# Kernel optimization log

Measured on AMD Instinct MI355X. Metric: run time of the kernel, lower is better.

## Reference

```python
import jax, jax.numpy as jnp
import numpy as np

# Geometry constants matching PointLoss.__init__ defaults
FOV_H = 360.0   # horizontal FOV (deg)
FOV_VU = 3.0    # upper vertical FOV (deg)
DH = 0.5        # delta_h
DV = 0.5        # delta_v
PROJ_H = 52     # int(26 / 0.5)
PROJ_W = 720    # int(360 / 0.5)
THETAC = 0.5    # confidence threshold
LAMDA = 1.0     # fov-loss weight
ANGRATE = 1.0   # anglelossrate
EPS = 1e-8


def setup_inputs() -> dict:
    key = jax.random.key(0)
    ks = jax.random.split(key, 10)
    B, H, W = 64, PROJ_H, PROJ_W
    return {
        "vertexmap_proj": jax.random.normal(ks[0], (B, H, W, 3), jnp.float32),
        "normalmap_proj": jax.random.normal(ks[1], (B, H, W, 3), jnp.float32),
        "uncertainty": jax.random.uniform(ks[2], (B, H, W), jnp.float32),
        "now_normalmap": jax.random.normal(ks[3], (B, H, W, 3), jnp.float32),
        "now_confidencemap": jax.random.uniform(ks[4], (B, H, W), jnp.float32),
        "last_normalmap": jax.random.normal(ks[5], (B, H, W, 3), jnp.float32),
        "last_vertexmap": jax.random.normal(ks[6], (B, H, W, 3), jnp.float32),
        "sx": jnp.zeros((1,), jnp.float32),
        "sq": jnp.zeros((1,), jnp.float32),
        "now_maskmap": jax.random.randint(ks[7], (B, H, W), 0, 2, jnp.int32),
        "last_maskmap": jax.random.randint(ks[8], (B, H, W), 0, 2, jnp.int32),
    }


def _gather_proj(m, flat_idx, B, H, W):
    """Gather pixels of m [B,H,W,(C)] at flat index [B,H,W] -> same shape as m."""
    if m.ndim == 3:
        mf = m.reshape(B, H * W)
        return jnp.take_along_axis(mf, flat_idx.reshape(B, H * W), axis=1).reshape(B, H, W)
    C = m.shape[-1]
    mf = m.reshape(B, H * W, C)
    idx = jnp.broadcast_to(flat_idx.reshape(B, H * W, 1), (B, H * W, C))
    return jnp.take_along_axis(mf, idx, axis=1).reshape(B, H, W, C)


def reference(vertexmap_proj, normalmap_proj, uncertainty, now_normalmap,
              now_confidencemap, last_normalmap, last_vertexmap, sx, sq,
              now_maskmap, last_maskmap):
    B, H, W, _ = vertexmap_proj.shape
    v = vertexmap_proj

    # mask of valid current pixels: maskmap > 0 and normal non-zero
    mask0 = (now_maskmap > 0) & (jnp.sum(jnp.abs(now_normalmap), -1) != 0)

    # spherical re-projection (movegrid=True)
    depth = jnp.sqrt(jnp.sum(v * v, -1) + EPS)
    yaw = jnp.arctan2(v[..., 1], v[..., 0]) * (180.0 / np.pi)
    pitch = jnp.arcsin(jnp.clip(v[..., 2] / depth, -1.0, 1.0)) * (180.0 / np.pi)
    proj_x = (FOV_H / 2 - yaw) / DH
    proj_y = (FOV_VU - pitch) / DV

    # fov loss = masked mse(proj, clamp(proj)) (F.mse_loss default mean)
    m0 = mask0.astype(v.dtype)
    n0 = jnp.maximum(jnp.sum(m0), 1.0)
    fovloss = (jnp.sum(m0 * (proj_x - jnp.clip(proj_x, 0, W - 1)) ** 2)
               + jnp.sum(m0 * (proj_y - jnp.clip(proj_y, 0, H - 1)) ** 2)) / n0

    prx = jnp.round(proj_x)
    pry = jnp.round(proj_y)
    inb = (prx >= 0) & (prx < W) & (pry >= 0) & (pry < H)
    prxi = jnp.clip(prx, 0, W - 1).astype(jnp.int32)
    pryi = jnp.clip(pry, 0, H - 1).astype(jnp.int32)
    flat = pryi * W + prxi  # [B,H,W]

    nl = _gather_proj(last_normalmap, flat, B, H, W)   # last normal at projected pixel
    vl = _gather_proj(last_vertexmap, flat, B, H, W)   # last vertex at projected pixel
    lm = _gather_proj(last_maskmap, flat, B, H, W)

    lastmask = (lm > 0) & (jnp.sum(jnp.abs(nl), -1) != 0)
    mask = mask0 & inb & lastmask & (now_confidencemap >= THETAC)
    m = mask.astype(v.dtype)
    n = jnp.maximum(jnp.sum(m), 1.0)

    # point-to-plane ICP residual, uncertainty-weighted L1
    r = jnp.sum(nl * (v - vl), -1)
    icploss = jnp.sum(m * uncertainty * jnp.abs(r)) / n

    # angular loss: 1 - |cos(angle between normals)|
    nn = normalmap_proj
    cosang = jnp.abs(jnp.sum(nl * nn, -1)) / jnp.sqrt(
        jnp.sum(nl * nl, -1) * jnp.sum(nn * nn, -1) + EPS)
    angloss = jnp.sum(m * uncertainty * (1.0 - cosang)) / n

    sx0, sq0 = sx[0], sq[0]
    total = (jnp.exp(-sx0) * icploss + sx0
             + ANGRATE * jnp.exp(-sq0) * angloss + sq0
             + LAMDA * fovloss)
    return total
```

## Files before the change

### kernel.cpp

```cpp
#include <hip/hip_runtime.h>
#include <math.h>


namespace {
constexpr int B_ = 64, H_ = 52, W_ = 720;
constexpr int HW_ = H_ * W_;
constexpr int NPIX = B_ * HW_;
constexpr int QPI  = HW_ / 4;
constexpr int NQUAD = NPIX / 4;
constexpr int NTHREADS = 256;
constexpr int NBLOCKS = NQUAD / NTHREADS;
constexpr float EPSF = 1e-8f;
constexpr float RAD2DEG = 57.29577951308232f;
}
static_assert(NBLOCKS * NTHREADS == NQUAD, "grid must tile quads exactly");

__global__ __launch_bounds__(NTHREADS) void pointloss_main(
    const float* __restrict__ v,
    const float* __restrict__ nrm,
    const float* __restrict__ unc,
    const float* __restrict__ nown,
    const float* __restrict__ conf,
    const float* __restrict__ lastn,
    const float* __restrict__ lastv,
    const int*   __restrict__ nowm,
    const int*   __restrict__ lastm,
    float* __restrict__ partials)
{
    float s_m0 = 0.f, s_fov = 0.f, s_m = 0.f, s_icp = 0.f, s_ang = 0.f;

    const float4* __restrict__ v4 = (const float4*)v;
    const float4* __restrict__ n4 = (const float4*)nown;
    const float4* __restrict__ r4 = (const float4*)nrm;
    const float4* __restrict__ u4 = (const float4*)unc;
    const int4*   __restrict__ m4 = (const int4*)nowm;
    const float4* __restrict__ c4 = (const float4*)conf;

    const int q  = blockIdx.x * NTHREADS + threadIdx.x;
    const int gbase = (q / QPI) * HW_;

    const float4 va = v4[3*q+0], vb = v4[3*q+1], vc = v4[3*q+2];
    const float4 na = n4[3*q+0], nb = n4[3*q+1], nc = n4[3*q+2];
    const int4   mm = m4[q];
    const float4 cf = c4[q];

    const float vx[4] = {va.x, va.w, vb.z, vc.y};
    const float vy[4] = {va.y, vb.x, vb.w, vc.z};
    const float vz[4] = {va.z, vb.y, vc.x, vc.w};
    const float ax[4] = {na.x, na.w, nb.z, nc.y};
    const float ay[4] = {na.y, nb.x, nb.w, nc.z};
    const float az[4] = {na.z, nb.y, nc.x, nc.w};
    const int   mk[4] = {mm.x, mm.y, mm.z, mm.w};
    const float cv[4] = {cf.x, cf.y, cf.z, cf.w};

    bool g[4];
    int  gi[4];
    #pragma unroll
    for (int j = 0; j < 4; ++j) {
        const bool mask0 = (mk[j] > 0) &&
            ((fabsf(ax[j]) + fabsf(ay[j]) + fabsf(az[j])) != 0.0f);

        const float depth = sqrtf(vx[j]*vx[j] + vy[j]*vy[j] + vz[j]*vz[j] + EPSF);
        const float yaw   = atan2f(vy[j], vx[j]) * RAD2DEG;
        const float pitch = asinf(fminf(fmaxf(vz[j] / depth, -1.f), 1.f)) * RAD2DEG;
        const float px = (180.0f - yaw) * 2.0f;
        const float py = (3.0f - pitch) * 2.0f;

        if (mask0) {
            const float dx = px - fminf(fmaxf(px, 0.f), (float)(W_ - 1));
            const float dy = py - fminf(fmaxf(py, 0.f), (float)(H_ - 1));
            s_m0  += 1.0f;
            s_fov += dx*dx + dy*dy;
        }

        const float prx = rintf(px), pry = rintf(py);
        const bool inb = (prx >= 0.f) && (prx < (float)W_) &&
                         (pry >= 0.f) && (pry < (float)H_);
        g[j]  = mask0 && inb && (cv[j] >= 0.5f);
        gi[j] = g[j] ? (gbase + (int)pry * W_ + (int)prx) : 0;
    }
    const bool anyg = g[0] | g[1] | g[2] | g[3];

    float4 ra = {0,0,0,0}, rb = {0,0,0,0}, rc = {0,0,0,0}, uq = {0,0,0,0};
    if (anyg) {
        ra = r4[3*q+0]; rb = r4[3*q+1]; rc = r4[3*q+2];
        uq = u4[q];
    }
    float lx[4] = {0,0,0,0}, ly[4] = {0,0,0,0}, lz[4] = {0,0,0,0};
    float wx[4] = {0,0,0,0}, wy[4] = {0,0,0,0}, wz[4] = {0,0,0,0};
    int   lm[4] = {0,0,0,0};
    #pragma unroll
    for (int j = 0; j < 4; ++j) {
        if (g[j]) {
            const int gi3 = 3 * gi[j];
            lx[j] = lastn[gi3+0]; ly[j] = lastn[gi3+1]; lz[j] = lastn[gi3+2];
            lm[j] = lastm[gi[j]];
            wx[j] = lastv[gi3+0]; wy[j] = lastv[gi3+1]; wz[j] = lastv[gi3+2];
        }
    }

    const float nx[4] = {ra.x, ra.w, rb.z, rc.y};
    const float ny[4] = {ra.y, rb.x, rb.w, rc.z};
    const float nz[4] = {ra.z, rb.y, rc.x, rc.w};
    const float uu[4] = {uq.x, uq.y, uq.z, uq.w};

    #pragma unroll
    for (int j = 0; j < 4; ++j) {
        if (g[j] && (lm[j] > 0) &&
            ((fabsf(lx[j]) + fabsf(ly[j]) + fabsf(lz[j])) != 0.f)) {
            const float r  = lx[j]*(vx[j]-wx[j]) + ly[j]*(vy[j]-wy[j])
                           + lz[j]*(vz[j]-wz[j]);
            const float dt = lx[j]*nx[j] + ly[j]*ny[j] + lz[j]*nz[j];
            const float den = (lx[j]*lx[j] + ly[j]*ly[j] + lz[j]*lz[j]) *
                              (nx[j]*nx[j] + ny[j]*ny[j] + nz[j]*nz[j]) + EPSF;
            const float cosang = fabsf(dt) * rsqrtf(den);
            s_m   += 1.0f;
            s_icp += uu[j] * fabsf(r);
            s_ang += uu[j] * (1.0f - cosang);
        }
    }

    #pragma unroll
    for (int off = 32; off > 0; off >>= 1) {
        s_m0  += __shfl_down(s_m0,  off);
        s_fov += __shfl_down(s_fov, off);
        s_m   += __shfl_down(s_m,   off);
        s_icp += __shfl_down(s_icp, off);
        s_ang += __shfl_down(s_ang, off);
    }
    __shared__ float red[NTHREADS / 64][5];
    const int lane = threadIdx.x & 63;
    const int wv   = threadIdx.x >> 6;
    if (lane == 0) {
        red[wv][0] = s_m0;  red[wv][1] = s_fov; red[wv][2] = s_m;
        red[wv][3] = s_icp; red[wv][4] = s_ang;
    }
    __syncthreads();
    if (threadIdx.x == 0) {
        float t[5] = {0.f, 0.f, 0.f, 0.f, 0.f};
        for (int w2 = 0; w2 < NTHREADS / 64; ++w2)
            for (int c = 0; c < 5; ++c) t[c] += red[w2][c];
        float* o = partials + blockIdx.x * 5;
        for (int c = 0; c < 5; ++c) o[c] = t[c];
    }
}

__global__ __launch_bounds__(256) void pointloss_finalize(
    const float* __restrict__ partials,
    const float* __restrict__ sx,
    const float* __restrict__ sq,
    float* __restrict__ out)
{
    double a0 = 0, a1 = 0, a2 = 0, a3 = 0, a4 = 0;
    for (int i = threadIdx.x; i < NBLOCKS; i += 256) {
        const float* pp = partials + i * 5;
        a0 += (double)pp[0]; a1 += (double)pp[1]; a2 += (double)pp[2];
        a3 += (double)pp[3]; a4 += (double)pp[4];
    }
    #pragma unroll
    for (int off = 32; off > 0; off >>= 1) {
        a0 += __shfl_down(a0, off);
        a1 += __shfl_down(a1, off);
        a2 += __shfl_down(a2, off);
        a3 += __shfl_down(a3, off);
        a4 += __shfl_down(a4, off);
    }
    __shared__ double red[4][5];
    const int lane = threadIdx.x & 63;
    const int wv   = threadIdx.x >> 6;
    if (lane == 0) {
        red[wv][0] = a0; red[wv][1] = a1; red[wv][2] = a2;
        red[wv][3] = a3; red[wv][4] = a4;
    }
    __syncthreads();
    if (threadIdx.x == 0) {
        double t[5] = {0, 0, 0, 0, 0};
        for (int w2 = 0; w2 < 4; ++w2)
            for (int c = 0; c < 5; ++c) t[c] += red[w2][c];
        const double n0 = fmax(t[0], 1.0);
        const double n  = fmax(t[2], 1.0);
        const double sx0 = (double)sx[0], sq0 = (double)sq[0];
        const double total = exp(-sx0) * (t[3] / n) + sx0
                           + exp(-sq0) * (t[4] / n) + sq0
                           + t[1] / n0;
        out[0] = (float)total;
    }
}

extern "C" void kernel_launch(void* const* d_in, const int* in_sizes, int n_in,
                              void* d_out, int out_size, void* d_ws, size_t ws_size,
                              hipStream_t stream) {
    const float* v     = (const float*)d_in[0];
    const float* nrm   = (const float*)d_in[1];
    const float* unc   = (const float*)d_in[2];
    const float* nown  = (const float*)d_in[3];
    const float* conf  = (const float*)d_in[4];
    const float* lastn = (const float*)d_in[5];
    const float* lastv = (const float*)d_in[6];
    const float* sx    = (const float*)d_in[7];
    const float* sq    = (const float*)d_in[8];
    const int*   nowm  = (const int*)d_in[9];
    const int*   lastm = (const int*)d_in[10];

    float* partials = (float*)d_ws;

    pointloss_main<<<NBLOCKS, NTHREADS, 0, stream>>>(
        v, nrm, unc, nown, conf, lastn, lastv, nowm, lastm, partials);
    pointloss_finalize<<<1, 256, 0, stream>>>(partials, sx, sq, (float*)d_out);
}
```

Before: 197.3 us.

## Process four quads per thread with register prefetch of next quad's streamed inputs

Each thread now handles four quads strided across the grid and loads the next quad's vertex, normal, mask and confidence vectors before computing the current one. This software pipelining is meant to hide global-load latency behind the trig-heavy projection math, and it cuts the block count and partial-sum count by four. The cost is higher register pressure, which may lower occupancy, and less parallelism to hide the latency of the data-dependent gathers.

```diff
diff --git a/kernel.cpp b/kernel.cpp
--- a/kernel.cpp
+++ b/kernel.cpp
@@ -9,11 +9,20 @@
 constexpr int QPI  = HW_ / 4;
 constexpr int NQUAD = NPIX / 4;
 constexpr int NTHREADS = 256;
-constexpr int NBLOCKS = NQUAD / NTHREADS;
+constexpr int QPT = 4;
+constexpr int NBLOCKS = NQUAD / (NTHREADS * QPT);
+constexpr int TSTRIDE = NBLOCKS * NTHREADS;
 constexpr float EPSF = 1e-8f;
 constexpr float RAD2DEG = 57.29577951308232f;
 }
-static_assert(NBLOCKS * NTHREADS == NQUAD, "grid must tile quads exactly");
+static_assert(NBLOCKS * NTHREADS * QPT == NQUAD, "grid must tile quads exactly");
+
+struct Stream {
+    float4 va, vb, vc;
+    float4 na, nb, nc;
+    int4   mm;
+    float4 cf;
+};
 
 __global__ __launch_bounds__(NTHREADS) void pointloss_main(
     const float* __restrict__ v,
@@ -36,88 +45,105 @@
     const int4*   __restrict__ m4 = (const int4*)nowm;
     const float4* __restrict__ c4 = (const float4*)conf;
 
-    const int q  = blockIdx.x * NTHREADS + threadIdx.x;
-    const int gbase = (q / QPI) * HW_;
-
-    const float4 va = v4[3*q+0], vb = v4[3*q+1], vc = v4[3*q+2];
-    const float4 na = n4[3*q+0], nb = n4[3*q+1], nc = n4[3*q+2];
-    const int4   mm = m4[q];
-    const float4 cf = c4[q];
-
-    const float vx[4] = {va.x, va.w, vb.z, vc.y};
-    const float vy[4] = {va.y, vb.x, vb.w, vc.z};
-    const float vz[4] = {va.z, vb.y, vc.x, vc.w};
-    const float ax[4] = {na.x, na.w, nb.z, nc.y};
-    const float ay[4] = {na.y, nb.x, nb.w, nc.z};
-    const float az[4] = {na.z, nb.y, nc.x, nc.w};
-    const int   mk[4] = {mm.x, mm.y, mm.z, mm.w};
-    const float cv[4] = {cf.x, cf.y, cf.z, cf.w};
-
-    bool g[4];
-    int  gi[4];
+    const int tid = blockIdx.x * NTHREADS + threadIdx.x;
+
+    auto ld = [&](int q) {
+        Stream s;
+        s.va = v4[3*q+0]; s.vb = v4[3*q+1]; s.vc = v4[3*q+2];
+        s.na = n4[3*q+0]; s.nb = n4[3*q+1]; s.nc = n4[3*q+2];
+        s.mm = m4[q];
+        s.cf = c4[q];
+        return s;
+    };
+
+    Stream s = ld(tid);
+
     #pragma unroll
-    for (int j = 0; j < 4; ++j) {
-        const bool mask0 = (mk[j] > 0) &&
-            ((fabsf(ax[j]) + fabsf(ay[j]) + fabsf(az[j])) != 0.0f);
-
-        const float depth = sqrtf(vx[j]*vx[j] + vy[j]*vy[j] + vz[j]*vz[j] + EPSF);
-        const float yaw   = atan2f(vy[j], vx[j]) * RAD2DEG;
-        const float pitch = asinf(fminf(fmaxf(vz[j] / depth, -1.f), 1.f)) * RAD2DEG;
-        const float px = (180.0f - yaw) * 2.0f;
-        const float py = (3.0f - pitch) * 2.0f;
-
-        if (mask0) {
-            const float dx = px - fminf(fmaxf(px, 0.f), (float)(W_ - 1));
-            const float dy = py - fminf(fmaxf(py, 0.f), (float)(H_ - 1));
-            s_m0  += 1.0f;
-            s_fov += dx*dx + dy*dy;
-        }
-
-        const float prx = rintf(px), pry = rintf(py);
-        const bool inb = (prx >= 0.f) && (prx < (float)W_) &&
-                         (pry >= 0.f) && (pry < (float)H_);
-        g[j]  = mask0 && inb && (cv[j] >= 0.5f);
-        gi[j] = g[j] ? (gbase + (int)pry * W_ + (int)prx) : 0;
-    }
-    const bool anyg = g[0] | g[1] | g[2] | g[3];
-
-    float4 ra = {0,0,0,0}, rb = {0,0,0,0}, rc = {0,0,0,0}, uq = {0,0,0,0};
-    if (anyg) {
-        ra = r4[3*q+0]; rb = r4[3*q+1]; rc = r4[3*q+2];
-        uq = u4[q];
-    }
-    float lx[4] = {0,0,0,0}, ly[4] = {0,0,0,0}, lz[4] = {0,0,0,0};
-    float wx[4] = {0,0,0,0}, wy[4] = {0,0,0,0}, wz[4] = {0,0,0,0};
-    int   lm[4] = {0,0,0,0};
-    #pragma unroll
-    for (int j = 0; j < 4; ++j) {
-        if (g[j]) {
-            const int gi3 = 3 * gi[j];
-            lx[j] = lastn[gi3+0]; ly[j] = lastn[gi3+1]; lz[j] = lastn[gi3+2];
-            lm[j] = lastm[gi[j]];
-            wx[j] = lastv[gi3+0]; wy[j] = lastv[gi3+1]; wz[j] = lastv[gi3+2];
-        }
-    }
-
-    const float nx[4] = {ra.x, ra.w, rb.z, rc.y};
-    const float ny[4] = {ra.y, rb.x, rb.w, rc.z};
-    const float nz[4] = {ra.z, rb.y, rc.x, rc.w};
-    const float uu[4] = {uq.x, uq.y, uq.z, uq.w};
-
-    #pragma unroll
-    for (int j = 0; j < 4; ++j) {
-        if (g[j] && (lm[j] > 0) &&
-            ((fabsf(lx[j]) + fabsf(ly[j]) + fabsf(lz[j])) != 0.f)) {
-            const float r  = lx[j]*(vx[j]-wx[j]) + ly[j]*(vy[j]-wy[j])
-                           + lz[j]*(vz[j]-wz[j]);
-            const float dt = lx[j]*nx[j] + ly[j]*ny[j] + lz[j]*nz[j];
-            const float den = (lx[j]*lx[j] + ly[j]*ly[j] + lz[j]*lz[j]) *
-                              (nx[j]*nx[j] + ny[j]*ny[j] + nz[j]*nz[j]) + EPSF;
-            const float cosang = fabsf(dt) * rsqrtf(den);
-            s_m   += 1.0f;
-            s_icp += uu[j] * fabsf(r);
-            s_ang += uu[j] * (1.0f - cosang);
-        }
+    for (int it = 0; it < QPT; ++it) {
+        const int q = tid + it * TSTRIDE;
+
+        Stream snext;
+        if (it < QPT - 1) snext = ld(q + TSTRIDE);
+
+        const int gbase = (q / QPI) * HW_;
+
+        const float vx[4] = {s.va.x, s.va.w, s.vb.z, s.vc.y};
+        const float vy[4] = {s.va.y, s.vb.x, s.vb.w, s.vc.z};
+        const float vz[4] = {s.va.z, s.vb.y, s.vc.x, s.vc.w};
+        const float ax[4] = {s.na.x, s.na.w, s.nb.z, s.nc.y};
+        const float ay[4] = {s.na.y, s.nb.x, s.nb.w, s.nc.z};
+        const float az[4] = {s.na.z, s.nb.y, s.nc.x, s.nc.w};
+        const int   mk[4] = {s.mm.x, s.mm.y, s.mm.z, s.mm.w};
+        const float cv[4] = {s.cf.x, s.cf.y, s.cf.z, s.cf.w};
+
+        bool g[4];
+        int  gi[4];
+        #pragma unroll
+        for (int j = 0; j < 4; ++j) {
+            const bool mask0 = (mk[j] > 0) &&
+                ((fabsf(ax[j]) + fabsf(ay[j]) + fabsf(az[j])) != 0.0f);
+
+            const float depth = sqrtf(vx[j]*vx[j] + vy[j]*vy[j] + vz[j]*vz[j] + EPSF);
+            const float yaw   = atan2f(vy[j], vx[j]) * RAD2DEG;
+            const float pitch = asinf(fminf(fmaxf(vz[j] / depth, -1.f), 1.f)) * RAD2DEG;
+            const float px = (180.0f - yaw) * 2.0f;
+            const float py = (3.0f - pitch) * 2.0f;
+
+            if (mask0) {
+                const float dx = px - fminf(fmaxf(px, 0.f), (float)(W_ - 1));
+                const float dy = py - fminf(fmaxf(py, 0.f), (float)(H_ - 1));
+                s_m0  += 1.0f;
+                s_fov += dx*dx + dy*dy;
+            }
+
+            const float prx = rintf(px), pry = rintf(py);
+            const bool inb = (prx >= 0.f) && (prx < (float)W_) &&
+                             (pry >= 0.f) && (pry < (float)H_);
+            g[j]  = mask0 && inb && (cv[j] >= 0.5f);
+            gi[j] = g[j] ? (gbase + (int)pry * W_ + (int)prx) : 0;
+        }
+        const bool anyg = g[0] | g[1] | g[2] | g[3];
+
+        float4 ra = {0,0,0,0}, rb = {0,0,0,0}, rc = {0,0,0,0}, uq = {0,0,0,0};
+        if (anyg) {
+            ra = r4[3*q+0]; rb = r4[3*q+1]; rc = r4[3*q+2];
+            uq = u4[q];
+        }
+        float lx[4] = {0,0,0,0}, ly[4] = {0,0,0,0}, lz[4] = {0,0,0,0};
+        float wx[4] = {0,0,0,0}, wy[4] = {0,0,0,0}, wz[4] = {0,0,0,0};
+        int   lm[4] = {0,0,0,0};
+        #pragma unroll
+        for (int j = 0; j < 4; ++j) {
+            if (g[j]) {
+                const int gi3 = 3 * gi[j];
+                lx[j] = lastn[gi3+0]; ly[j] = lastn[gi3+1]; lz[j] = lastn[gi3+2];
+                lm[j] = lastm[gi[j]];
+                wx[j] = lastv[gi3+0]; wy[j] = lastv[gi3+1]; wz[j] = lastv[gi3+2];
+            }
+        }
+
+        const float nx[4] = {ra.x, ra.w, rb.z, rc.y};
+        const float ny[4] = {ra.y, rb.x, rb.w, rc.z};
+        const float nz[4] = {ra.z, rb.y, rc.x, rc.w};
+        const float uu[4] = {uq.x, uq.y, uq.z, uq.w};
+
+        #pragma unroll
+        for (int j = 0; j < 4; ++j) {
+            if (g[j] && (lm[j] > 0) &&
+                ((fabsf(lx[j]) + fabsf(ly[j]) + fabsf(lz[j])) != 0.f)) {
+                const float r  = lx[j]*(vx[j]-wx[j]) + ly[j]*(vy[j]-wy[j])
+                               + lz[j]*(vz[j]-wz[j]);
+                const float dt = lx[j]*nx[j] + ly[j]*ny[j] + lz[j]*nz[j];
+                const float den = (lx[j]*lx[j] + ly[j]*ly[j] + lz[j]*lz[j]) *
+                                  (nx[j]*nx[j] + ny[j]*ny[j] + nz[j]*nz[j]) + EPSF;
+                const float cosang = fabsf(dt) * rsqrtf(den);
+                s_m   += 1.0f;
+                s_icp += uu[j] * fabsf(r);
+                s_ang += uu[j] * (1.0f - cosang);
+            }
+        }
+
+        s = snext;
     }
 
     #pragma unroll
```

After: 199.1 us. About the same (+0.9%).

## Compact valid pixels into a workspace queue and gather last-frame data separately

Applied to the files above, without the earlier changes.

The main kernel no longer does the divergent random gathers from the last-frame maps. Instead it uses wave ballots and one atomic per wave to append compact 32-byte records for valid pixels to a workspace buffer. A second grid-stride kernel reads those records, performs the gathers and computes the ICP and angle partial sums, and the finalize kernel merges both sets of partials. This aims to remove lane divergence and wasted gather slots in the main pass. In exchange it adds a memset, an extra launch and extra write/read traffic, and records beyond the workspace capacity are silently dropped.

```diff
diff --git a/kernel.cpp b/kernel.cpp
--- a/kernel.cpp
+++ b/kernel.cpp
@@ -8,26 +8,33 @@
 constexpr int NPIX = B_ * HW_;
 constexpr int QPI  = HW_ / 4;
 constexpr int NQUAD = NPIX / 4;
-constexpr int NTHREADS = 256;
-constexpr int NBLOCKS = NQUAD / NTHREADS;
+constexpr int NT = 256;
+constexpr int NB1 = NQUAD / NT;
+constexpr int NB2 = 1024;
 constexpr float EPSF = 1e-8f;
 constexpr float RAD2DEG = 57.29577951308232f;
-}
-static_assert(NBLOCKS * NTHREADS == NQUAD, "grid must tile quads exactly");
-
-__global__ __launch_bounds__(NTHREADS) void pointloss_main(
+
+constexpr size_t WS_COUNTER = 0;
+constexpr size_t WS_P1      = 16;
+constexpr size_t WS_P2      = 20480;
+constexpr size_t WS_RECS    = 65536;
+}
+static_assert(NB1 * NT == NQUAD, "grid must tile quads exactly");
+
+
+__global__ __launch_bounds__(NT) void pointloss_main(
     const float* __restrict__ v,
     const float* __restrict__ nrm,
     const float* __restrict__ unc,
     const float* __restrict__ nown,
     const float* __restrict__ conf,
-    const float* __restrict__ lastn,
-    const float* __restrict__ lastv,
     const int*   __restrict__ nowm,
-    const int*   __restrict__ lastm,
-    float* __restrict__ partials)
+    unsigned int* __restrict__ counter,
+    float* __restrict__ p1,
+    float4* __restrict__ recs,
+    int cap)
 {
-    float s_m0 = 0.f, s_fov = 0.f, s_m = 0.f, s_icp = 0.f, s_ang = 0.f;
+    float s_m0 = 0.f, s_fov = 0.f;
 
     const float4* __restrict__ v4 = (const float4*)v;
     const float4* __restrict__ n4 = (const float4*)nown;
@@ -36,7 +43,7 @@
     const int4*   __restrict__ m4 = (const int4*)nowm;
     const float4* __restrict__ c4 = (const float4*)conf;
 
-    const int q  = blockIdx.x * NTHREADS + threadIdx.x;
+    const int q = blockIdx.x * NT + threadIdx.x;
     const int gbase = (q / QPI) * HW_;
 
     const float4 va = v4[3*q+0], vb = v4[3*q+1], vc = v4[3*q+2];
@@ -86,76 +93,136 @@
         ra = r4[3*q+0]; rb = r4[3*q+1]; rc = r4[3*q+2];
         uq = u4[q];
     }
-    float lx[4] = {0,0,0,0}, ly[4] = {0,0,0,0}, lz[4] = {0,0,0,0};
-    float wx[4] = {0,0,0,0}, wy[4] = {0,0,0,0}, wz[4] = {0,0,0,0};
-    int   lm[4] = {0,0,0,0};
-    #pragma unroll
-    for (int j = 0; j < 4; ++j) {
-        if (g[j]) {
-            const int gi3 = 3 * gi[j];
-            lx[j] = lastn[gi3+0]; ly[j] = lastn[gi3+1]; lz[j] = lastn[gi3+2];
-            lm[j] = lastm[gi[j]];
-            wx[j] = lastv[gi3+0]; wy[j] = lastv[gi3+1]; wz[j] = lastv[gi3+2];
-        }
-    }
-
     const float nx[4] = {ra.x, ra.w, rb.z, rc.y};
     const float ny[4] = {ra.y, rb.x, rb.w, rc.z};
     const float nz[4] = {ra.z, rb.y, rc.x, rc.w};
     const float uu[4] = {uq.x, uq.y, uq.z, uq.w};
 
+    const int lane = threadIdx.x & 63;
+    const unsigned long long lt = ((unsigned long long)1 << lane) - 1ull;
+    unsigned long long bal[4];
+    int tj[4], tot = 0;
     #pragma unroll
     for (int j = 0; j < 4; ++j) {
-        if (g[j] && (lm[j] > 0) &&
-            ((fabsf(lx[j]) + fabsf(ly[j]) + fabsf(lz[j])) != 0.f)) {
-            const float r  = lx[j]*(vx[j]-wx[j]) + ly[j]*(vy[j]-wy[j])
-                           + lz[j]*(vz[j]-wz[j]);
-            const float dt = lx[j]*nx[j] + ly[j]*ny[j] + lz[j]*nz[j];
-            const float den = (lx[j]*lx[j] + ly[j]*ly[j] + lz[j]*lz[j]) *
-                              (nx[j]*nx[j] + ny[j]*ny[j] + nz[j]*nz[j]) + EPSF;
+        bal[j] = __ballot(g[j]);
+        tj[j]  = __popcll(bal[j]);
+        tot   += tj[j];
+    }
+    int base = 0;
+    if (lane == 0 && tot > 0)
+        base = (int)atomicAdd(counter, (unsigned int)tot);
+    base = __shfl(base, 0);
+
+    int off = base;
+    #pragma unroll
+    for (int j = 0; j < 4; ++j) {
+        if (g[j]) {
+            const int idx = off + __popcll(bal[j] & lt);
+            if (idx < cap) {
+                float4 r0, r1;
+                r0.x = __int_as_float(gi[j]);
+                r0.y = uu[j]; r0.z = vx[j]; r0.w = vy[j];
+                r1.x = vz[j]; r1.y = nx[j]; r1.z = ny[j]; r1.w = nz[j];
+                recs[2*idx+0] = r0;
+                recs[2*idx+1] = r1;
+            }
+        }
+        off += tj[j];
+    }
+
+    #pragma unroll
+    for (int o = 32; o > 0; o >>= 1) {
+        s_m0  += __shfl_down(s_m0,  o);
+        s_fov += __shfl_down(s_fov, o);
+    }
+    __shared__ float red[NT / 64][2];
+    const int wv = threadIdx.x >> 6;
+    if (lane == 0) { red[wv][0] = s_m0; red[wv][1] = s_fov; }
+    __syncthreads();
+    if (threadIdx.x == 0) {
+        float t0 = 0.f, t1 = 0.f;
+        for (int w2 = 0; w2 < NT / 64; ++w2) { t0 += red[w2][0]; t1 += red[w2][1]; }
+        p1[blockIdx.x * 2 + 0] = t0;
+        p1[blockIdx.x * 2 + 1] = t1;
+    }
+}
+
+__global__ __launch_bounds__(NT) void pointloss_gather(
+    const float* __restrict__ lastn,
+    const float* __restrict__ lastv,
+    const int*   __restrict__ lastm,
+    const unsigned int* __restrict__ counter,
+    const float4* __restrict__ recs,
+    int cap,
+    float* __restrict__ p2)
+{
+    float s_m = 0.f, s_icp = 0.f, s_ang = 0.f;
+    const int n = min((int)*counter, cap);
+    const int stride = NB2 * NT;
+
+    for (int i = blockIdx.x * NT + threadIdx.x; i < n; i += stride) {
+        const float4 r0 = recs[2*i+0];
+        const float4 r1 = recs[2*i+1];
+        const int   gi = __float_as_int(r0.x);
+        const float u  = r0.y;
+        const float vx = r0.z, vy = r0.w, vz = r1.x;
+        const float nx = r1.y, ny = r1.z, nz = r1.w;
+
+        const int gi3 = 3 * gi;
+        const int   lmv = lastm[gi];
+        const float lx = lastn[gi3+0], ly = lastn[gi3+1], lz = lastn[gi3+2];
+        const float wx = lastv[gi3+0], wy = lastv[gi3+1], wz = lastv[gi3+2];
+
+        if ((lmv > 0) && ((fabsf(lx) + fabsf(ly) + fabsf(lz)) != 0.f)) {
+            const float r  = lx*(vx-wx) + ly*(vy-wy) + lz*(vz-wz);
+            const float dt = lx*nx + ly*ny + lz*nz;
+            const float den = (lx*lx + ly*ly + lz*lz) *
+                              (nx*nx + ny*ny + nz*nz) + EPSF;
             const float cosang = fabsf(dt) * rsqrtf(den);
             s_m   += 1.0f;
-            s_icp += uu[j] * fabsf(r);
-            s_ang += uu[j] * (1.0f - cosang);
-        }
-    }
-
-    #pragma unroll
-    for (int off = 32; off > 0; off >>= 1) {
-        s_m0  += __shfl_down(s_m0,  off);
-        s_fov += __shfl_down(s_fov, off);
-        s_m   += __shfl_down(s_m,   off);
-        s_icp += __shfl_down(s_icp, off);
-        s_ang += __shfl_down(s_ang, off);
-    }
-    __shared__ float red[NTHREADS / 64][5];
+            s_icp += u * fabsf(r);
+            s_ang += u * (1.0f - cosang);
+        }
+    }
+
+    #pragma unroll
+    for (int o = 32; o > 0; o >>= 1) {
+        s_m   += __shfl_down(s_m,   o);
+        s_icp += __shfl_down(s_icp, o);
+        s_ang += __shfl_down(s_ang, o);
+    }
+    __shared__ float red[NT / 64][3];
     const int lane = threadIdx.x & 63;
     const int wv   = threadIdx.x >> 6;
-    if (lane == 0) {
-        red[wv][0] = s_m0;  red[wv][1] = s_fov; red[wv][2] = s_m;
-        red[wv][3] = s_icp; red[wv][4] = s_ang;
-    }
+    if (lane == 0) { red[wv][0] = s_m; red[wv][1] = s_icp; red[wv][2] = s_ang; }
     __syncthreads();
     if (threadIdx.x == 0) {
-        float t[5] = {0.f, 0.f, 0.f, 0.f, 0.f};
-        for (int w2 = 0; w2 < NTHREADS / 64; ++w2)
-            for (int c = 0; c < 5; ++c) t[c] += red[w2][c];
-        float* o = partials + blockIdx.x * 5;
-        for (int c = 0; c < 5; ++c) o[c] = t[c];
+        float t0 = 0.f, t1 = 0.f, t2 = 0.f;
+        for (int w2 = 0; w2 < NT / 64; ++w2) {
+            t0 += red[w2][0]; t1 += red[w2][1]; t2 += red[w2][2];
+        }
+        p2[blockIdx.x * 3 + 0] = t0;
+        p2[blockIdx.x * 3 + 1] = t1;
+        p2[blockIdx.x * 3 + 2] = t2;
     }
 }
 
 __global__ __launch_bounds__(256) void pointloss_finalize(
-    const float* __restrict__ partials,
+    const float* __restrict__ p1,
+    const float* __restrict__ p2,
     const float* __restrict__ sx,
     const float* __restrict__ sq,
     float* __restrict__ out)
 {
     double a0 = 0, a1 = 0, a2 = 0, a3 = 0, a4 = 0;
-    for (int i = threadIdx.x; i < NBLOCKS; i += 256) {
-        const float* pp = partials + i * 5;
-        a0 += (double)pp[0]; a1 += (double)pp[1]; a2 += (double)pp[2];
-        a3 += (double)pp[3]; a4 += (double)pp[4];
+    for (int i = threadIdx.x; i < NB1; i += 256) {
+        a0 += (double)p1[i*2+0];
+        a1 += (double)p1[i*2+1];
+    }
+    for (int i = threadIdx.x; i < NB2; i += 256) {
+        a2 += (double)p2[i*3+0];
+        a3 += (double)p2[i*3+1];
+        a4 += (double)p2[i*3+2];
     }
     #pragma unroll
     for (int off = 32; off > 0; off >>= 1) {
@@ -202,9 +269,18 @@
     const int*   nowm  = (const int*)d_in[9];
     const int*   lastm = (const int*)d_in[10];
 
-    float* partials = (float*)d_ws;
-
-    pointloss_main<<<NBLOCKS, NTHREADS, 0, stream>>>(
-        v, nrm, unc, nown, conf, lastn, lastv, nowm, lastm, partials);
-    pointloss_finalize<<<1, 256, 0, stream>>>(partials, sx, sq, (float*)d_out);
-}
+    char* ws = (char*)d_ws;
+    unsigned int* counter = (unsigned int*)(ws + WS_COUNTER);
+    float*  p1   = (float*)(ws + WS_P1);
+    float*  p2   = (float*)(ws + WS_P2);
+    float4* recs = (float4*)(ws + WS_RECS);
+    const int cap = (int)(((ws_size > WS_RECS ? ws_size - WS_RECS : 0)) / 32);
+
+    hipMemsetAsync(counter, 0, sizeof(unsigned int), stream);
+
+    pointloss_main<<<NB1, NT, 0, stream>>>(
+        v, nrm, unc, nown, conf, nowm, counter, p1, recs, cap);
+    pointloss_gather<<<NB2, NT, 0, stream>>>(
+        lastn, lastv, lastm, counter, recs, cap, p2);
+    pointloss_finalize<<<1, 256, 0, stream>>>(p1, p2, sx, sq, (float*)d_out);
+}
```

New measurement: 283.4 us. +43.6%, slower.

## Stage AoS loads through LDS, shrink grid with scalar tail, split gather batches

Applied to the files above, without the earlier changes.

Loads of the 3-component vertex and normal arrays are made fully coalesced by having each thread read consecutive float4s and then transposing them through shared memory. The grid is cut to a fixed 2048 blocks, and the pixels left over are handled by a scalar per-thread tail path. The projection math now runs while the normal data is being staged. The random gathers are issued in two batches of two pixels to limit register pressure under the new launch bound of 8. The costs are extra barriers, shared-memory traffic and an uncoalesced scalar tail.

```diff
diff --git a/kernel.cpp b/kernel.cpp
--- a/kernel.cpp
+++ b/kernel.cpp
@@ -8,14 +8,16 @@
 constexpr int NPIX = B_ * HW_;
 constexpr int QPI  = HW_ / 4;
 constexpr int NQUAD = NPIX / 4;
-constexpr int NTHREADS = 256;
-constexpr int NBLOCKS = NQUAD / NTHREADS;
+constexpr int NT = 256;
+constexpr int NB = 2048;
+constexpr int NTHR = NB * NT;
+constexpr int PTAIL0 = NTHR * 4;
 constexpr float EPSF = 1e-8f;
 constexpr float RAD2DEG = 57.29577951308232f;
 }
-static_assert(NBLOCKS * NTHREADS == NQUAD, "grid must tile quads exactly");
-
-__global__ __launch_bounds__(NTHREADS) void pointloss_main(
+static_assert(NTHR <= NQUAD, "quad phase must not overrun");
+
+__global__ __launch_bounds__(NT, 8) void pointloss_main(
     const float* __restrict__ v,
     const float* __restrict__ nrm,
     const float* __restrict__ unc,
@@ -36,17 +38,50 @@
     const int4*   __restrict__ m4 = (const int4*)nowm;
     const float4* __restrict__ c4 = (const float4*)conf;
 
-    const int q  = blockIdx.x * NTHREADS + threadIdx.x;
-    const int gbase = (q / QPI) * HW_;
-
-    const float4 va = v4[3*q+0], vb = v4[3*q+1], vc = v4[3*q+2];
-    const float4 na = n4[3*q+0], nb = n4[3*q+1], nc = n4[3*q+2];
+    const int t  = threadIdx.x;
+    const int qb = blockIdx.x * NT;
+    const int q  = qb + t;
+
+    __shared__ float4 lds[3 * NT];
+
+    const float4 sv0 = v4[3*qb + t], sv1 = v4[3*qb + NT + t], sv2 = v4[3*qb + 2*NT + t];
+    const float4 sn0 = n4[3*qb + t], sn1 = n4[3*qb + NT + t], sn2 = n4[3*qb + 2*NT + t];
     const int4   mm = m4[q];
     const float4 cf = c4[q];
+
+    lds[t] = sv0; lds[t + NT] = sv1; lds[t + 2*NT] = sv2;
+    __syncthreads();
+    const float4 va = lds[3*t+0], vb = lds[3*t+1], vc = lds[3*t+2];
+    __syncthreads();
+    lds[t] = sn0; lds[t + NT] = sn1; lds[t + 2*NT] = sn2;
 
     const float vx[4] = {va.x, va.w, vb.z, vc.y};
     const float vy[4] = {va.y, vb.x, vb.w, vc.z};
     const float vz[4] = {va.z, vb.y, vc.x, vc.w};
+    const int gbase = (q / QPI) * HW_;
+
+    float dxy2[4];
+    int   gidx[4];
+    bool  inb[4];
+    #pragma unroll
+    for (int j = 0; j < 4; ++j) {
+        const float depth = sqrtf(vx[j]*vx[j] + vy[j]*vy[j] + vz[j]*vz[j] + EPSF);
+        const float yaw   = atan2f(vy[j], vx[j]) * RAD2DEG;
+        const float pitch = asinf(fminf(fmaxf(vz[j] / depth, -1.f), 1.f)) * RAD2DEG;
+        const float px = (180.0f - yaw) * 2.0f;
+        const float py = (3.0f - pitch) * 2.0f;
+        const float dx = px - fminf(fmaxf(px, 0.f), (float)(W_ - 1));
+        const float dy = py - fminf(fmaxf(py, 0.f), (float)(H_ - 1));
+        dxy2[j] = dx*dx + dy*dy;
+        const float prx = rintf(px), pry = rintf(py);
+        inb[j]  = (prx >= 0.f) && (prx < (float)W_) &&
+                  (pry >= 0.f) && (pry < (float)H_);
+        gidx[j] = inb[j] ? (gbase + (int)pry * W_ + (int)prx) : 0;
+    }
+
+    __syncthreads();
+    const float4 na = lds[3*t+0], nb = lds[3*t+1], nc = lds[3*t+2];
+
     const float ax[4] = {na.x, na.w, nb.z, nc.y};
     const float ay[4] = {na.y, nb.x, nb.w, nc.z};
     const float az[4] = {na.z, nb.y, nc.x, nc.w};
@@ -54,30 +89,12 @@
     const float cv[4] = {cf.x, cf.y, cf.z, cf.w};
 
     bool g[4];
-    int  gi[4];
     #pragma unroll
     for (int j = 0; j < 4; ++j) {
         const bool mask0 = (mk[j] > 0) &&
             ((fabsf(ax[j]) + fabsf(ay[j]) + fabsf(az[j])) != 0.0f);
-
-        const float depth = sqrtf(vx[j]*vx[j] + vy[j]*vy[j] + vz[j]*vz[j] + EPSF);
-        const float yaw   = atan2f(vy[j], vx[j]) * RAD2DEG;
-        const float pitch = asinf(fminf(fmaxf(vz[j] / depth, -1.f), 1.f)) * RAD2DEG;
-        const float px = (180.0f - yaw) * 2.0f;
-        const float py = (3.0f - pitch) * 2.0f;
-
-        if (mask0) {
-            const float dx = px - fminf(fmaxf(px, 0.f), (float)(W_ - 1));
-            const float dy = py - fminf(fmaxf(py, 0.f), (float)(H_ - 1));
-            s_m0  += 1.0f;
-            s_fov += dx*dx + dy*dy;
-        }
-
-        const float prx = rintf(px), pry = rintf(py);
-        const bool inb = (prx >= 0.f) && (prx < (float)W_) &&
-                         (pry >= 0.f) && (pry < (float)H_);
-        g[j]  = mask0 && inb && (cv[j] >= 0.5f);
-        gi[j] = g[j] ? (gbase + (int)pry * W_ + (int)prx) : 0;
+        if (mask0) { s_m0 += 1.0f; s_fov += dxy2[j]; }
+        g[j] = mask0 && inb[j] && (cv[j] >= 0.5f);
     }
     const bool anyg = g[0] | g[1] | g[2] | g[3];
 
@@ -86,62 +103,113 @@
         ra = r4[3*q+0]; rb = r4[3*q+1]; rc = r4[3*q+2];
         uq = u4[q];
     }
-    float lx[4] = {0,0,0,0}, ly[4] = {0,0,0,0}, lz[4] = {0,0,0,0};
-    float wx[4] = {0,0,0,0}, wy[4] = {0,0,0,0}, wz[4] = {0,0,0,0};
-    int   lm[4] = {0,0,0,0};
-    #pragma unroll
-    for (int j = 0; j < 4; ++j) {
-        if (g[j]) {
-            const int gi3 = 3 * gi[j];
-            lx[j] = lastn[gi3+0]; ly[j] = lastn[gi3+1]; lz[j] = lastn[gi3+2];
-            lm[j] = lastm[gi[j]];
-            wx[j] = lastv[gi3+0]; wy[j] = lastv[gi3+1]; wz[j] = lastv[gi3+2];
+    const float nxx[4] = {ra.x, ra.w, rb.z, rc.y};
+    const float nyy[4] = {ra.y, rb.x, rb.w, rc.z};
+    const float nzz[4] = {ra.z, rb.y, rc.x, rc.w};
+    const float uu[4]  = {uq.x, uq.y, uq.z, uq.w};
+
+    #pragma unroll
+    for (int jp = 0; jp < 2; ++jp) {
+        float lx[2], ly[2], lz[2], wx[2], wy[2], wz[2];
+        int   lm2[2];
+        #pragma unroll
+        for (int k = 0; k < 2; ++k) {
+            const int j = 2*jp + k;
+            lx[k] = 0.f; ly[k] = 0.f; lz[k] = 0.f;
+            wx[k] = 0.f; wy[k] = 0.f; wz[k] = 0.f; lm2[k] = 0;
+            if (g[j]) {
+                const int gi3 = 3 * gidx[j];
+                lx[k] = lastn[gi3+0]; ly[k] = lastn[gi3+1]; lz[k] = lastn[gi3+2];
+                lm2[k] = lastm[gidx[j]];
+                wx[k] = lastv[gi3+0]; wy[k] = lastv[gi3+1]; wz[k] = lastv[gi3+2];
+            }
         }
-    }
-
-    const float nx[4] = {ra.x, ra.w, rb.z, rc.y};
-    const float ny[4] = {ra.y, rb.x, rb.w, rc.z};
-    const float nz[4] = {ra.z, rb.y, rc.x, rc.w};
-    const float uu[4] = {uq.x, uq.y, uq.z, uq.w};
-
-    #pragma unroll
-    for (int j = 0; j < 4; ++j) {
-        if (g[j] && (lm[j] > 0) &&
-            ((fabsf(lx[j]) + fabsf(ly[j]) + fabsf(lz[j])) != 0.f)) {
-            const float r  = lx[j]*(vx[j]-wx[j]) + ly[j]*(vy[j]-wy[j])
-                           + lz[j]*(vz[j]-wz[j]);
-            const float dt = lx[j]*nx[j] + ly[j]*ny[j] + lz[j]*nz[j];
-            const float den = (lx[j]*lx[j] + ly[j]*ly[j] + lz[j]*lz[j]) *
-                              (nx[j]*nx[j] + ny[j]*ny[j] + nz[j]*nz[j]) + EPSF;
-            const float cosang = fabsf(dt) * rsqrtf(den);
-            s_m   += 1.0f;
-            s_icp += uu[j] * fabsf(r);
-            s_ang += uu[j] * (1.0f - cosang);
+        #pragma unroll
+        for (int k = 0; k < 2; ++k) {
+            const int j = 2*jp + k;
+            if (g[j] && (lm2[k] > 0) &&
+                ((fabsf(lx[k]) + fabsf(ly[k]) + fabsf(lz[k])) != 0.f)) {
+                const float r  = lx[k]*(vx[j]-wx[k]) + ly[k]*(vy[j]-wy[k])
+                               + lz[k]*(vz[j]-wz[k]);
+                const float dt = lx[k]*nxx[j] + ly[k]*nyy[j] + lz[k]*nzz[j];
+                const float den = (lx[k]*lx[k] + ly[k]*ly[k] + lz[k]*lz[k]) *
+                                  (nxx[j]*nxx[j] + nyy[j]*nyy[j] + nzz[j]*nzz[j]) + EPSF;
+                const float cosang = fabsf(dt) * rsqrtf(den);
+                s_m   += 1.0f;
+                s_icp += uu[j] * fabsf(r);
+                s_ang += uu[j] * (1.0f - cosang);
+            }
         }
     }
 
-    #pragma unroll
-    for (int off = 32; off > 0; off >>= 1) {
-        s_m0  += __shfl_down(s_m0,  off);
-        s_fov += __shfl_down(s_fov, off);
-        s_m   += __shfl_down(s_m,   off);
-        s_icp += __shfl_down(s_icp, off);
-        s_ang += __shfl_down(s_ang, off);
-    }
-    __shared__ float red[NTHREADS / 64][5];
-    const int lane = threadIdx.x & 63;
-    const int wv   = threadIdx.x >> 6;
+    {
+        const int p = PTAIL0 + qb + t;
+        if (p < NPIX) {
+            const float tvx = v[3*p+0], tvy = v[3*p+1], tvz = v[3*p+2];
+            const float tax = nown[3*p+0], tay = nown[3*p+1], taz = nown[3*p+2];
+            const bool mask0 = (nowm[p] > 0) &&
+                ((fabsf(tax) + fabsf(tay) + fabsf(taz)) != 0.0f);
+
+            const float depth = sqrtf(tvx*tvx + tvy*tvy + tvz*tvz + EPSF);
+            const float yaw   = atan2f(tvy, tvx) * RAD2DEG;
+            const float pitch = asinf(fminf(fmaxf(tvz / depth, -1.f), 1.f)) * RAD2DEG;
+            const float px = (180.0f - yaw) * 2.0f;
+            const float py = (3.0f - pitch) * 2.0f;
+
+            if (mask0) {
+                const float dx = px - fminf(fmaxf(px, 0.f), (float)(W_ - 1));
+                const float dy = py - fminf(fmaxf(py, 0.f), (float)(H_ - 1));
+                s_m0  += 1.0f;
+                s_fov += dx*dx + dy*dy;
+            }
+
+            const float prx = rintf(px), pry = rintf(py);
+            const bool tinb = (prx >= 0.f) && (prx < (float)W_) &&
+                              (pry >= 0.f) && (pry < (float)H_);
+            if (mask0 && tinb && (conf[p] >= 0.5f)) {
+                const int gi = (p / HW_) * HW_ + (int)pry * W_ + (int)prx;
+                const int gi3 = 3 * gi;
+                const float lx = lastn[gi3+0], ly = lastn[gi3+1], lz = lastn[gi3+2];
+                if ((lastm[gi] > 0) && ((fabsf(lx) + fabsf(ly) + fabsf(lz)) != 0.f)) {
+                    const float u  = unc[p];
+                    const float wx = lastv[gi3+0], wy = lastv[gi3+1], wz = lastv[gi3+2];
+                    const float r  = lx*(tvx-wx) + ly*(tvy-wy) + lz*(tvz-wz);
+                    const float nx = nrm[3*p+0], ny = nrm[3*p+1], nz = nrm[3*p+2];
+                    const float dt = lx*nx + ly*ny + lz*nz;
+                    const float den = (lx*lx + ly*ly + lz*lz) *
+                                      (nx*nx + ny*ny + nz*nz) + EPSF;
+                    const float cosang = fabsf(dt) * rsqrtf(den);
+                    s_m   += 1.0f;
+                    s_icp += u * fabsf(r);
+                    s_ang += u * (1.0f - cosang);
+                }
+            }
+        }
+    }
+
+    #pragma unroll
+    for (int o = 32; o > 0; o >>= 1) {
+        s_m0  += __shfl_down(s_m0,  o);
+        s_fov += __shfl_down(s_fov, o);
+        s_m   += __shfl_down(s_m,   o);
+        s_icp += __shfl_down(s_icp, o);
+        s_ang += __shfl_down(s_ang, o);
+    }
+    __syncthreads();
+    float* red = (float*)lds;
+    const int lane = t & 63;
+    const int wv   = t >> 6;
     if (lane == 0) {
-        red[wv][0] = s_m0;  red[wv][1] = s_fov; red[wv][2] = s_m;
-        red[wv][3] = s_icp; red[wv][4] = s_ang;
-    }
-    __syncthreads();
-    if (threadIdx.x == 0) {
-        float t[5] = {0.f, 0.f, 0.f, 0.f, 0.f};
-        for (int w2 = 0; w2 < NTHREADS / 64; ++w2)
-            for (int c = 0; c < 5; ++c) t[c] += red[w2][c];
+        red[wv*5+0] = s_m0;  red[wv*5+1] = s_fov; red[wv*5+2] = s_m;
+        red[wv*5+3] = s_icp; red[wv*5+4] = s_ang;
+    }
+    __syncthreads();
+    if (t == 0) {
+        float acc[5] = {0.f, 0.f, 0.f, 0.f, 0.f};
+        for (int w2 = 0; w2 < NT / 64; ++w2)
+            for (int c = 0; c < 5; ++c) acc[c] += red[w2*5+c];
         float* o = partials + blockIdx.x * 5;
-        for (int c = 0; c < 5; ++c) o[c] = t[c];
+        for (int c = 0; c < 5; ++c) o[c] = acc[c];
     }
 }
 
@@ -152,7 +220,7 @@
     float* __restrict__ out)
 {
     double a0 = 0, a1 = 0, a2 = 0, a3 = 0, a4 = 0;
-    for (int i = threadIdx.x; i < NBLOCKS; i += 256) {
+    for (int i = threadIdx.x; i < NB; i += 256) {
         const float* pp = partials + i * 5;
         a0 += (double)pp[0]; a1 += (double)pp[1]; a2 += (double)pp[2];
         a3 += (double)pp[3]; a4 += (double)pp[4];
@@ -174,15 +242,15 @@
     }
     __syncthreads();
     if (threadIdx.x == 0) {
-        double t[5] = {0, 0, 0, 0, 0};
+        double tt[5] = {0, 0, 0, 0, 0};
         for (int w2 = 0; w2 < 4; ++w2)
-            for (int c = 0; c < 5; ++c) t[c] += red[w2][c];
-        const double n0 = fmax(t[0], 1.0);
-        const double n  = fmax(t[2], 1.0);
+            for (int c = 0; c < 5; ++c) tt[c] += red[w2][c];
+        const double n0 = fmax(tt[0], 1.0);
+        const double n  = fmax(tt[2], 1.0);
         const double sx0 = (double)sx[0], sq0 = (double)sq[0];
-        const double total = exp(-sx0) * (t[3] / n) + sx0
-                           + exp(-sq0) * (t[4] / n) + sq0
-                           + t[1] / n0;
+        const double total = exp(-sx0) * (tt[3] / n) + sx0
+                           + exp(-sq0) * (tt[4] / n) + sq0
+                           + tt[1] / n0;
         out[0] = (float)total;
     }
 }
@@ -204,7 +272,7 @@
 
     float* partials = (float*)d_ws;
 
-    pointloss_main<<<NBLOCKS, NTHREADS, 0, stream>>>(
+    pointloss_main<<<NB, NT, 0, stream>>>(
         v, nrm, unc, nown, conf, lastn, lastv, nowm, lastm, partials);
     pointloss_finalize<<<1, 256, 0, stream>>>(partials, sx, sq, (float*)d_out);
 }
```

New measurement: 195.0 us. Within noise of the previous version (-1.2%).
